# Kernel tuning notes

Hardware: AMD Instinct MI355X
Metric: run time of the kernel (lower is better)

The kernel has to match this reference:

```python
import jax, jax.numpy as jnp
import numpy as np
from jax import lax

T = 2048          # tokens (batch*seq, module flattens to [-1, hidden])
H = 2048          # hidden_size
E = 32            # n_routed_experts
DF = 1024         # moe_intermediate_size
DS = 4096         # moe_shared_expert_intermediate_size
TOP_K = 6         # num_experts_per_tok
N_GROUP = 8
TOPK_GROUP = 4
SCALE = 2.5       # routed_scaling_factor
NORM_TOPK = True


def relu2(x):
    r = jax.nn.relu(x)
    return r * r


def setup_inputs() -> dict:
    key = jax.random.key(0)
    ks = jax.random.split(key, 7)
    s = 0.02
    return {
        "x": jax.random.normal(ks[0], (T, H), dtype=jnp.float32),
        "router_w": jax.random.normal(ks[1], (E, H), dtype=jnp.float32) * s,
        "router_b": jax.random.normal(ks[2], (E,), dtype=jnp.float32) * s,
        "w_up": jax.random.normal(ks[3], (E, H, DF), dtype=jnp.float32) * s,
        "w_down": jax.random.normal(ks[4], (E, DF, H), dtype=jnp.float32) * s,
        "shared_up": jax.random.normal(ks[5], (H, DS), dtype=jnp.float32) * s,
        "shared_down": jax.random.normal(ks[6], (DS, H), dtype=jnp.float32) * s,
    }


def _route(x, router_w, router_b):
    # router in fp32: logits -> sigmoid scores -> group-restricted top-k
    logits = x @ router_w.T                                  # [T, E]
    scores = jax.nn.sigmoid(logits)
    sfc = scores + router_b[None, :]                         # scores_for_choice
    gsize = E // N_GROUP
    grp = sfc.reshape(T, N_GROUP, gsize)
    group_scores = lax.top_k(grp, 2)[0].sum(-1)              # [T, n_group] sum of top-2
    _, gidx = lax.top_k(group_scores, TOPK_GROUP)            # [T, topk_group]
    group_mask = jax.nn.one_hot(gidx, N_GROUP, dtype=sfc.dtype).sum(1)  # [T, n_group]
    score_mask = jnp.repeat(group_mask, gsize, axis=1)       # [T, E]
    masked = jnp.where(score_mask > 0, sfc, 0.0)
    _, tidx = lax.top_k(masked, TOP_K)                       # [T, top_k]
    tw = jnp.take_along_axis(scores, tidx, axis=1)           # gather raw scores
    if NORM_TOPK:
        tw = tw / (tw.sum(-1, keepdims=True) + 1e-20)
    tw = tw * SCALE
    return tidx, tw


def reference(x, router_w, router_b, w_up, w_down, shared_up, shared_down):
    tidx, tw = _route(x, router_w, router_b)
    # dense combine weights [T, E]; equals sum of routed weights per expert
    combine = (jax.nn.one_hot(tidx, E, dtype=tw.dtype) * tw[..., None]).sum(1)
    # routed experts (no bias, so scaling before down_proj == scaling the output)
    h = jnp.einsum('td,edf->tef', x, w_up)                   # [T, E, DF]
    a = relu2(h) * combine[:, :, None]
    moe_out = jnp.einsum('tef,efd->td', a, w_down)           # [T, H]
    shared_out = relu2(x @ shared_up) @ shared_down
    return moe_out + shared_out
```

## Files before the change

### kernel.cpp

```cpp
#include <hip/hip_runtime.h>
#include <hip/hip_bf16.h>
#include <math.h>

#define T_TOK 2048
#define HID   2048
#define NE    32
#define DF    1024
#define DSZ   4096
#define TOPK  6
#define NGRP  8
#define TOPKG 4
#define RSCALE 2.5f
#define EXT_E 36
#define NSLOT 20480

typedef __attribute__((ext_vector_type(8))) short short8;
typedef __attribute__((ext_vector_type(4))) float f32x4;

typedef __attribute__((address_space(1))) const void gv1;
typedef __attribute__((address_space(3))) void lv3;

static __device__ __forceinline__ void gload16(const void* g, void* l) {
    __builtin_amdgcn_global_load_lds((gv1*)g, (lv3*)l, 16, 0, 0);
}

static __device__ __forceinline__ unsigned short f2b(float f) {
    union { float f; unsigned u; } v; v.f = f;
    unsigned r = v.u + 0x7fffu + ((v.u >> 16) & 1u);
    return (unsigned short)(r >> 16);
}

__global__ __launch_bounds__(256)
void router_kernel(const float* __restrict__ x, const float* __restrict__ rw,
                   const float* __restrict__ rb,
                   int* __restrict__ tidx, float* __restrict__ tw,
                   int* __restrict__ counts, unsigned short* __restrict__ xb) {
    __shared__ float xs[HID];
    __shared__ float part[256];
    __shared__ float scores[NE];
    __shared__ float sfc[NE];
    int t = blockIdx.x;
    int tid = threadIdx.x;
    for (int i = tid; i < HID / 4; i += 256) {
        ((float4*)xs)[i] = ((const float4*)(x + (size_t)t * HID))[i];
    }
    __syncthreads();
    {
        float4 a = ((const float4*)xs)[tid * 2];
        float4 b = ((const float4*)xs)[tid * 2 + 1];
        short8 o;
        o[0] = (short)f2b(a.x); o[1] = (short)f2b(a.y); o[2] = (short)f2b(a.z); o[3] = (short)f2b(a.w);
        o[4] = (short)f2b(b.x); o[5] = (short)f2b(b.y); o[6] = (short)f2b(b.z); o[7] = (short)f2b(b.w);
        *(short8*)(xb + (size_t)t * HID + tid * 8) = o;
    }
    int e = tid & 31, ch = tid >> 5;
    const float* w = rw + (size_t)e * HID + ch * 256;
    const float* xv = xs + ch * 256;
    float p = 0.f;
    #pragma unroll 8
    for (int k = 0; k < 256; ++k) p += xv[k] * w[k];
    part[tid] = p;
    __syncthreads();
    if (tid < 32) {
        float l = 0.f;
        #pragma unroll
        for (int c = 0; c < 8; ++c) l += part[c * 32 + tid];
        float s = 1.f / (1.f + expf(-l));
        scores[tid] = s;
        sfc[tid] = s + rb[tid];
    }
    __syncthreads();
    if (tid == 0) {
        float gs[NGRP];
        for (int g = 0; g < NGRP; ++g) {
            float v[4];
            for (int i = 0; i < 4; ++i) v[i] = sfc[g * 4 + i];
            int bi = 0;
            for (int i = 1; i < 4; ++i) if (v[i] > v[bi]) bi = i;
            float m1 = v[bi]; v[bi] = -INFINITY;
            int bj = 0;
            for (int i = 1; i < 4; ++i) if (v[i] > v[bj]) bj = i;
            gs[g] = m1 + v[bj];
        }
        bool gsel[NGRP];
        for (int g = 0; g < NGRP; ++g) gsel[g] = false;
        for (int k = 0; k < TOPKG; ++k) {
            int bi = -1; float b = -INFINITY;
            for (int g = 0; g < NGRP; ++g)
                if (!gsel[g] && gs[g] > b) { b = gs[g]; bi = g; }
            gsel[bi] = true;
        }
        float masked[NE];
        for (int i = 0; i < NE; ++i) masked[i] = gsel[i >> 2] ? sfc[i] : 0.0f;
        int sel[TOPK]; float wv[TOPK]; float wsum = 0.f;
        for (int k = 0; k < TOPK; ++k) {
            int bi = -1; float b = -INFINITY;
            for (int i = 0; i < NE; ++i)
                if (masked[i] > b) { b = masked[i]; bi = i; }
            masked[bi] = -INFINITY;
            sel[k] = bi; wv[k] = scores[bi]; wsum += wv[k];
        }
        float inv = RSCALE / (wsum + 1e-20f);
        for (int k = 0; k < TOPK; ++k) {
            tidx[t * TOPK + k] = sel[k];
            tw[t * TOPK + k] = wv[k] * inv;
            atomicAdd(&counts[sel[k]], 1);
        }
    }
}

__global__ void scan_kernel(const int* __restrict__ counts, int* __restrict__ offsets) {
    if (threadIdx.x == 0) {
        int a = 0;
        for (int e2 = 0; e2 < NE; ++e2) { offsets[e2] = a; a += counts[e2]; }
        offsets[NE] = a;
        for (int j = 1; j <= 4; ++j) offsets[NE + j] = 12288 + j * T_TOK;
    }
}

__global__ void scatter_kernel(const int* __restrict__ tidx, const float* __restrict__ tw,
                               const int* __restrict__ offsets, int* __restrict__ cursors,
                               int* __restrict__ perm, float* __restrict__ pw,
                               int* __restrict__ slot_of) {
    int t = blockIdx.x * blockDim.x + threadIdx.x;
    if (t >= T_TOK) return;
    for (int k = 0; k < TOPK; ++k) {
        int e = tidx[t * TOPK + k];
        int pos = atomicAdd(&cursors[e], 1);
        int slot = offsets[e] + pos;
        perm[slot] = t;
        pw[slot] = tw[t * TOPK + k];
        slot_of[t * TOPK + k] = slot;
    }
    #pragma unroll
    for (int j = 0; j < 4; ++j) {
        int slot = 12288 + j * T_TOK + t;
        perm[slot] = t;
        pw[slot] = 1.0f;
    }
}

static __device__ __forceinline__ void transpose_tile_v2(
        const float* __restrict__ src, unsigned short* __restrict__ dst,
        int rs, int K, int k0, int n0) {
    __shared__ float tile_t[32][132];
    int t = threadIdx.x;
    int kk0 = t >> 3;
    int c4 = (t & 7) * 4;
    #pragma unroll
    for (int p = 0; p < 4; ++p) {
        int kk = kk0 + 32 * p;
        float4 v = *(const float4*)(src + (size_t)(k0 + kk) * rs + n0 + c4);
        tile_t[c4 + 0][kk] = v.x;
        tile_t[c4 + 1][kk] = v.y;
        tile_t[c4 + 2][kk] = v.z;
        tile_t[c4 + 3][kk] = v.w;
    }
    __syncthreads();
    int n = t >> 3;
    int kb = (t & 7) * 8;
    #pragma unroll
    for (int s = 0; s < 2; ++s) {
        int kc = kb + 64 * s;
        float4 a = *(const float4*)&tile_t[n][kc];
        float4 b = *(const float4*)&tile_t[n][kc + 4];
        short8 o;
        o[0] = (short)f2b(a.x); o[1] = (short)f2b(a.y); o[2] = (short)f2b(a.z); o[3] = (short)f2b(a.w);
        o[4] = (short)f2b(b.x); o[5] = (short)f2b(b.y); o[6] = (short)f2b(b.z); o[7] = (short)f2b(b.w);
        *(short8*)(dst + (size_t)(n0 + n) * K + k0 + kc) = o;
    }
}

__global__ __launch_bounds__(256)
void transpose_up_kernel(const float* __restrict__ w_up, const float* __restrict__ sh_up,
                         unsigned short* __restrict__ bufU) {
    int z = blockIdx.z;
    const float* src; int rs;
    if (z < NE) { src = w_up + (size_t)z * HID * DF; rs = DF; }
    else        { src = sh_up + (size_t)(z - NE) * DF; rs = DSZ; }
    transpose_tile_v2(src, bufU + (size_t)z * DF * HID, rs, HID,
                      blockIdx.y * 128, blockIdx.x * 32);
}

__global__ __launch_bounds__(256)
void transpose_dn_kernel(const float* __restrict__ w_dn, const float* __restrict__ sh_dn,
                         unsigned short* __restrict__ bufD) {
    int z = blockIdx.z;
    const float* src = (z < NE) ? (w_dn + (size_t)z * DF * HID)
                                : (sh_dn + (size_t)(z - NE) * DF * HID);
    transpose_tile_v2(src, bufD + (size_t)z * HID * DF, HID, DF,
                      blockIdx.y * 128, blockIdx.x * 32);
}

__global__ __launch_bounds__(256, 2)
void gemm_up_kernel(const unsigned short* __restrict__ xb, const unsigned short* __restrict__ bufU,
                    unsigned short* __restrict__ act, const int* __restrict__ offsets,
                    const int* __restrict__ perm, const float* __restrict__ pw) {
    constexpr int K = HID, N = DF;
    __shared__ __align__(16) char lds[32768];
    char* As = lds;
    char* Bs = lds + 16384;

    int tid = threadIdx.x;
    int lane = tid & 63, wvid = tid >> 6, wr = wvid >> 1, wc = wvid & 1;

    int bz = blockIdx.z;
    int off = offsets[bz], end = offsets[bz + 1];
    int row0 = off + blockIdx.y * 128;
    if (row0 >= end) return;
    int n0 = blockIdx.x * 128;

    int lr = lane >> 3;
    int csrc = (((lane & 7) ^ lr) << 4);
    size_t abyte[4], bbyte[4];
    int ldsoff[4];
    const char* Bb = (const char*)bufU + (size_t)bz * ((size_t)N * K * 2);
    #pragma unroll
    for (int p = 0; p < 4; ++p) {
        int r = p * 32 + wvid * 8 + lr;
        int gr = row0 + r;
        if (gr > end - 1) gr = end - 1;
        abyte[p] = (size_t)perm[gr] * (K * 2);
        bbyte[p] = (size_t)(n0 + r) * (K * 2);
        ldsoff[p] = (p * 32 + wvid * 8) * 128;
    }

    f32x4 acc[4][4] = {};
    for (int k0 = 0; k0 < K; k0 += 64) {
        __syncthreads();
        #pragma unroll
        for (int p = 0; p < 4; ++p) {
            gload16((const char*)xb + abyte[p] + k0 * 2 + csrc, As + ldsoff[p]);
            gload16(Bb + bbyte[p] + k0 * 2 + csrc, Bs + ldsoff[p]);
        }
        __syncthreads();
        #pragma unroll
        for (int ks = 0; ks < 2; ++ks) {
            int kg = lane >> 4, r16 = lane & 15;
            short8 af[4], bfr[4];
            #pragma unroll
            for (int m = 0; m < 4; ++m) {
                int r = wr * 64 + m * 16 + r16;
                af[m] = *(const short8*)(As + r * 128 + ((ks * 64 + kg * 16) ^ ((r & 7) << 4)));
            }
            #pragma unroll
            for (int n = 0; n < 4; ++n) {
                int c = wc * 64 + n * 16 + r16;
                bfr[n] = *(const short8*)(Bs + c * 128 + ((ks * 64 + kg * 16) ^ ((c & 7) << 4)));
            }
            #pragma unroll
            for (int m = 0; m < 4; ++m)
                #pragma unroll
                for (int n = 0; n < 4; ++n)
                    acc[m][n] = __builtin_amdgcn_mfma_f32_16x16x32_bf16(af[m], bfr[n], acc[m][n], 0, 0, 0);
        }
    }

    int r16 = lane & 15, rg = lane >> 4;
    #pragma unroll
    for (int m = 0; m < 4; ++m) {
        #pragma unroll
        for (int j = 0; j < 4; ++j) {
            int rr = row0 + wr * 64 + m * 16 + rg * 4 + j;
            if (rr < end) {
                float scale = pw[rr];
                #pragma unroll
                for (int n = 0; n < 4; ++n) {
                    int cc = n0 + wc * 64 + n * 16 + r16;
                    float v = acc[m][n][j];
                    v = v > 0.f ? v * v : 0.f;
                    act[(size_t)rr * N + cc] = f2b(v * scale);
                }
            }
        }
    }
}

__global__ __launch_bounds__(256, 2)
void gemm_down_kernel(const unsigned short* __restrict__ act, const unsigned short* __restrict__ bufD,
                      float* __restrict__ slotout, const int* __restrict__ offsets) {
    constexpr int K = DF, N = HID;
    __shared__ __align__(16) char lds[32768];
    char* As = lds;
    char* Bs = lds + 16384;

    int tid = threadIdx.x;
    int lane = tid & 63, wvid = tid >> 6, wr = wvid >> 1, wc = wvid & 1;

    int bz = blockIdx.z;
    int off = offsets[bz], end = offsets[bz + 1];
    int row0 = off + blockIdx.y * 128;
    if (row0 >= end) return;
    int n0 = blockIdx.x * 128;

    int lr = lane >> 3;
    int csrc = (((lane & 7) ^ lr) << 4);
    size_t abyte[4], bbyte[4];
    int ldsoff[4];
    const char* Bb = (const char*)bufD + (size_t)bz * ((size_t)N * K * 2);
    #pragma unroll
    for (int p = 0; p < 4; ++p) {
        int r = p * 32 + wvid * 8 + lr;
        int gr = row0 + r;
        if (gr > end - 1) gr = end - 1;
        abyte[p] = (size_t)gr * (K * 2);
        bbyte[p] = (size_t)(n0 + r) * (K * 2);
        ldsoff[p] = (p * 32 + wvid * 8) * 128;
    }

    f32x4 acc[4][4] = {};
    for (int k0 = 0; k0 < K; k0 += 64) {
        __syncthreads();
        #pragma unroll
        for (int p = 0; p < 4; ++p) {
            gload16((const char*)act + abyte[p] + k0 * 2 + csrc, As + ldsoff[p]);
            gload16(Bb + bbyte[p] + k0 * 2 + csrc, Bs + ldsoff[p]);
        }
        __syncthreads();
        #pragma unroll
        for (int ks = 0; ks < 2; ++ks) {
            int kg = lane >> 4, r16 = lane & 15;
            short8 af[4], bfr[4];
            #pragma unroll
            for (int m = 0; m < 4; ++m) {
                int r = wr * 64 + m * 16 + r16;
                af[m] = *(const short8*)(As + r * 128 + ((ks * 64 + kg * 16) ^ ((r & 7) << 4)));
            }
            #pragma unroll
            for (int n = 0; n < 4; ++n) {
                int c = wc * 64 + n * 16 + r16;
                bfr[n] = *(const short8*)(Bs + c * 128 + ((ks * 64 + kg * 16) ^ ((c & 7) << 4)));
            }
            #pragma unroll
            for (int m = 0; m < 4; ++m)
                #pragma unroll
                for (int n = 0; n < 4; ++n)
                    acc[m][n] = __builtin_amdgcn_mfma_f32_16x16x32_bf16(af[m], bfr[n], acc[m][n], 0, 0, 0);
        }
    }

    int r16 = lane & 15, rg = lane >> 4;
    #pragma unroll
    for (int m = 0; m < 4; ++m) {
        #pragma unroll
        for (int j = 0; j < 4; ++j) {
            int rr = row0 + wr * 64 + m * 16 + rg * 4 + j;
            if (rr < end) {
                #pragma unroll
                for (int n = 0; n < 4; ++n) {
                    int cc = n0 + wc * 64 + n * 16 + r16;
                    slotout[(size_t)rr * N + cc] = acc[m][n][j];
                }
            }
        }
    }
}

__global__ void combine_kernel(const float* __restrict__ slotout, const int* __restrict__ slot_of,
                               float* __restrict__ out) {
    int t = blockIdx.x, tid = threadIdx.x;
    int s[10];
    #pragma unroll
    for (int k = 0; k < TOPK; ++k) s[k] = slot_of[t * TOPK + k];
    #pragma unroll
    for (int j = 0; j < 4; ++j) s[TOPK + j] = 12288 + j * T_TOK + t;
    #pragma unroll
    for (int p = 0; p < 2; ++p) {
        int c = (p * 256 + tid) * 4;
        float4 a = {0.f, 0.f, 0.f, 0.f};
        #pragma unroll
        for (int k = 0; k < 10; ++k) {
            float4 v = *(const float4*)(slotout + (size_t)s[k] * HID + c);
            a.x += v.x; a.y += v.y; a.z += v.z; a.w += v.w;
        }
        *(float4*)(out + (size_t)t * HID + c) = a;
    }
}

extern "C" void kernel_launch(void* const* d_in, const int* in_sizes, int n_in,
                              void* d_out, int out_size, void* d_ws, size_t ws_size,
                              hipStream_t stream) {
    const float* x     = (const float*)d_in[0];
    const float* rw    = (const float*)d_in[1];
    const float* rb    = (const float*)d_in[2];
    const float* w_up  = (const float*)d_in[3];
    const float* w_dn  = (const float*)d_in[4];
    const float* sh_up = (const float*)d_in[5];
    const float* sh_dn = (const float*)d_in[6];
    float* out = (float*)d_out;
    char* ws = (char*)d_ws;

    int*   counts  = (int*)(ws);
    int*   cursors = (int*)(ws + 128);
    int*   offsets = (int*)(ws + 256);
    int*   tidx    = (int*)(ws + 1024);
    float* tw      = (float*)(ws + 50176);
    int*   slot_of = (int*)(ws + 99328);
    int*   perm    = (int*)(ws + 148480);
    float* pw      = (float*)(ws + 230400);
    unsigned short* xb   = (unsigned short*)(ws + 312320);
    unsigned short* act  = (unsigned short*)(ws + 8700928);
    unsigned short* bufU = (unsigned short*)(ws + 50643968);
    unsigned short* bufD = (unsigned short*)(ws + 201638912);
    float* slotout       = (float*)(ws + 352633856);

    hipMemsetAsync(ws, 0, 256, stream);

    router_kernel<<<T_TOK, 256, 0, stream>>>(x, rw, rb, tidx, tw, counts, xb);
    scan_kernel<<<1, 64, 0, stream>>>(counts, offsets);
    scatter_kernel<<<(T_TOK + 255) / 256, 256, 0, stream>>>(tidx, tw, offsets, cursors,
                                                            perm, pw, slot_of);

    transpose_up_kernel<<<dim3(32, 16, EXT_E), 256, 0, stream>>>(w_up, sh_up, bufU);
    gemm_up_kernel<<<dim3(DF / 128, T_TOK / 128, EXT_E), 256, 0, stream>>>(
        xb, bufU, act, offsets, perm, pw);

    transpose_dn_kernel<<<dim3(64, 8, EXT_E), 256, 0, stream>>>(w_dn, sh_dn, bufD);
    gemm_down_kernel<<<dim3(HID / 128, T_TOK / 128, EXT_E), 256, 0, stream>>>(
        act, bufD, slotout, offsets);

    combine_kernel<<<T_TOK, 256, 0, stream>>>(slotout, slot_of, out);
}
```

Baseline: 600.5 us.

## Double-buffer LDS in MoE GEMMs and rewrite weight transpose without shared memory

```diff
diff --git a/kernel.cpp b/kernel.cpp
--- a/kernel.cpp
+++ b/kernel.cpp
@@ -140,34 +140,19 @@
     }
 }
 
-static __device__ __forceinline__ void transpose_tile_v2(
+static __device__ __forceinline__ void transpose_col32(
         const float* __restrict__ src, unsigned short* __restrict__ dst,
-        int rs, int K, int k0, int n0) {
-    __shared__ float tile_t[32][132];
-    int t = threadIdx.x;
-    int kk0 = t >> 3;
-    int c4 = (t & 7) * 4;
-    #pragma unroll
-    for (int p = 0; p < 4; ++p) {
-        int kk = kk0 + 32 * p;
-        float4 v = *(const float4*)(src + (size_t)(k0 + kk) * rs + n0 + c4);
-        tile_t[c4 + 0][kk] = v.x;
-        tile_t[c4 + 1][kk] = v.y;
-        tile_t[c4 + 2][kk] = v.z;
-        tile_t[c4 + 3][kk] = v.w;
-    }
-    __syncthreads();
-    int n = t >> 3;
-    int kb = (t & 7) * 8;
-    #pragma unroll
-    for (int s = 0; s < 2; ++s) {
-        int kc = kb + 64 * s;
-        float4 a = *(const float4*)&tile_t[n][kc];
-        float4 b = *(const float4*)&tile_t[n][kc + 4];
+        int rs, int K, int k0, int n) {
+    float v[32];
+    #pragma unroll
+    for (int p = 0; p < 32; ++p)
+        v[p] = src[(size_t)(k0 + p) * rs + n];
+    #pragma unroll
+    for (int q = 0; q < 4; ++q) {
         short8 o;
-        o[0] = (short)f2b(a.x); o[1] = (short)f2b(a.y); o[2] = (short)f2b(a.z); o[3] = (short)f2b(a.w);
-        o[4] = (short)f2b(b.x); o[5] = (short)f2b(b.y); o[6] = (short)f2b(b.z); o[7] = (short)f2b(b.w);
-        *(short8*)(dst + (size_t)(n0 + n) * K + k0 + kc) = o;
+        #pragma unroll
+        for (int i = 0; i < 8; ++i) o[i] = (short)f2b(v[q * 8 + i]);
+        *(short8*)(dst + (size_t)n * K + k0 + q * 8) = o;
     }
 }
 
@@ -178,8 +163,8 @@
     const float* src; int rs;
     if (z < NE) { src = w_up + (size_t)z * HID * DF; rs = DF; }
     else        { src = sh_up + (size_t)(z - NE) * DF; rs = DSZ; }
-    transpose_tile_v2(src, bufU + (size_t)z * DF * HID, rs, HID,
-                      blockIdx.y * 128, blockIdx.x * 32);
+    transpose_col32(src, bufU + (size_t)z * DF * HID, rs, HID,
+                    blockIdx.y * 32, blockIdx.x * 256 + threadIdx.x);
 }
 
 __global__ __launch_bounds__(256)
@@ -188,8 +173,8 @@
     int z = blockIdx.z;
     const float* src = (z < NE) ? (w_dn + (size_t)z * DF * HID)
                                 : (sh_dn + (size_t)(z - NE) * DF * HID);
-    transpose_tile_v2(src, bufD + (size_t)z * HID * DF, HID, DF,
-                      blockIdx.y * 128, blockIdx.x * 32);
+    transpose_col32(src, bufD + (size_t)z * HID * DF, HID, DF,
+                    blockIdx.y * 32, blockIdx.x * 256 + threadIdx.x);
 }
 
 __global__ __launch_bounds__(256, 2)
@@ -197,9 +182,7 @@
                     unsigned short* __restrict__ act, const int* __restrict__ offsets,
                     const int* __restrict__ perm, const float* __restrict__ pw) {
     constexpr int K = HID, N = DF;
-    __shared__ __align__(16) char lds[32768];
-    char* As = lds;
-    char* Bs = lds + 16384;
+    __shared__ __align__(16) char lds[65536];
 
     int tid = threadIdx.x;
     int lane = tid & 63, wvid = tid >> 6, wr = wvid >> 1, wc = wvid & 1;
@@ -226,14 +209,27 @@
     }
 
     f32x4 acc[4][4] = {};
-    for (int k0 = 0; k0 < K; k0 += 64) {
-        __syncthreads();
-        #pragma unroll
-        for (int p = 0; p < 4; ++p) {
-            gload16((const char*)xb + abyte[p] + k0 * 2 + csrc, As + ldsoff[p]);
-            gload16(Bb + bbyte[p] + k0 * 2 + csrc, Bs + ldsoff[p]);
-        }
-        __syncthreads();
+    constexpr int NT = K / 64;
+    int cur = 0;
+    #pragma unroll
+    for (int p = 0; p < 4; ++p) {
+        gload16((const char*)xb + abyte[p] + csrc, lds + ldsoff[p]);
+        gload16(Bb + bbyte[p] + csrc, lds + 16384 + ldsoff[p]);
+    }
+    __syncthreads();
+
+    for (int t = 0; t < NT; ++t) {
+        char* As = lds + cur * 32768;
+        char* Bs = As + 16384;
+        if (t + 1 < NT) {
+            int k2 = (t + 1) * 128;
+            char* Ad = lds + (cur ^ 1) * 32768;
+            #pragma unroll
+            for (int p = 0; p < 4; ++p) {
+                gload16((const char*)xb + abyte[p] + k2 + csrc, Ad + ldsoff[p]);
+                gload16(Bb + bbyte[p] + k2 + csrc, Ad + 16384 + ldsoff[p]);
+            }
+        }
         #pragma unroll
         for (int ks = 0; ks < 2; ++ks) {
             int kg = lane >> 4, r16 = lane & 15;
@@ -254,6 +250,8 @@
                 for (int n = 0; n < 4; ++n)
                     acc[m][n] = __builtin_amdgcn_mfma_f32_16x16x32_bf16(af[m], bfr[n], acc[m][n], 0, 0, 0);
         }
+        __syncthreads();
+        cur ^= 1;
     }
 
     int r16 = lane & 15, rg = lane >> 4;
@@ -280,9 +278,7 @@
 void gemm_down_kernel(const unsigned short* __restrict__ act, const unsigned short* __restrict__ bufD,
                       float* __restrict__ slotout, const int* __restrict__ offsets) {
     constexpr int K = DF, N = HID;
-    __shared__ __align__(16) char lds[32768];
-    char* As = lds;
-    char* Bs = lds + 16384;
+    __shared__ __align__(16) char lds[65536];
 
     int tid = threadIdx.x;
     int lane = tid & 63, wvid = tid >> 6, wr = wvid >> 1, wc = wvid & 1;
@@ -309,14 +305,27 @@
     }
 
     f32x4 acc[4][4] = {};
-    for (int k0 = 0; k0 < K; k0 += 64) {
-        __syncthreads();
-        #pragma unroll
-        for (int p = 0; p < 4; ++p) {
-            gload16((const char*)act + abyte[p] + k0 * 2 + csrc, As + ldsoff[p]);
-            gload16(Bb + bbyte[p] + k0 * 2 + csrc, Bs + ldsoff[p]);
-        }
-        __syncthreads();
+    constexpr int NT = K / 64;
+    int cur = 0;
+    #pragma unroll
+    for (int p = 0; p < 4; ++p) {
+        gload16((const char*)act + abyte[p] + csrc, lds + ldsoff[p]);
+        gload16(Bb + bbyte[p] + csrc, lds + 16384 + ldsoff[p]);
+    }
+    __syncthreads();
+
+    for (int t = 0; t < NT; ++t) {
+        char* As = lds + cur * 32768;
+        char* Bs = As + 16384;
+        if (t + 1 < NT) {
+            int k2 = (t + 1) * 128;
+            char* Ad = lds + (cur ^ 1) * 32768;
+            #pragma unroll
+            for (int p = 0; p < 4; ++p) {
+                gload16((const char*)act + abyte[p] + k2 + csrc, Ad + ldsoff[p]);
+                gload16(Bb + bbyte[p] + k2 + csrc, Ad + 16384 + ldsoff[p]);
+            }
+        }
         #pragma unroll
         for (int ks = 0; ks < 2; ++ks) {
             int kg = lane >> 4, r16 = lane & 15;
@@ -337,6 +346,8 @@
                 for (int n = 0; n < 4; ++n)
                     acc[m][n] = __builtin_amdgcn_mfma_f32_16x16x32_bf16(af[m], bfr[n], acc[m][n], 0, 0, 0);
         }
+        __syncthreads();
+        cur ^= 1;
     }
 
     int r16 = lane & 15, rg = lane >> 4;
@@ -411,11 +422,11 @@
     scatter_kernel<<<(T_TOK + 255) / 256, 256, 0, stream>>>(tidx, tw, offsets, cursors,
                                                             perm, pw, slot_of);
 
-    transpose_up_kernel<<<dim3(32, 16, EXT_E), 256, 0, stream>>>(w_up, sh_up, bufU);
+    transpose_up_kernel<<<dim3(DF / 256, HID / 32, EXT_E), 256, 0, stream>>>(w_up, sh_up, bufU);
     gemm_up_kernel<<<dim3(DF / 128, T_TOK / 128, EXT_E), 256, 0, stream>>>(
         xb, bufU, act, offsets, perm, pw);
 
-    transpose_dn_kernel<<<dim3(64, 8, EXT_E), 256, 0, stream>>>(w_dn, sh_dn, bufD);
+    transpose_dn_kernel<<<dim3(HID / 256, DF / 32, EXT_E), 256, 0, stream>>>(w_dn, sh_dn, bufD);
     gemm_down_kernel<<<dim3(HID / 128, T_TOK / 128, EXT_E), 256, 0, stream>>>(
         act, bufD, slotout, offsets);
 
```

Result: slower. 726.5 us (+21.0%).

## Merge weight transposes into one kernel and store down-proj slot outputs as bf16

Applied to the files above, without the earlier changes.

```diff
diff --git a/kernel.cpp b/kernel.cpp
--- a/kernel.cpp
+++ b/kernel.cpp
@@ -28,6 +28,11 @@
     union { float f; unsigned u; } v; v.f = f;
     unsigned r = v.u + 0x7fffu + ((v.u >> 16) & 1u);
     return (unsigned short)(r >> 16);
+}
+
+static __device__ __forceinline__ float b2f(unsigned short b) {
+    union { float f; unsigned u; } v; v.u = ((unsigned)b) << 16;
+    return v.f;
 }
 
 __global__ __launch_bounds__(256)
@@ -140,56 +145,52 @@
     }
 }
 
-static __device__ __forceinline__ void transpose_tile_v2(
+static __device__ __forceinline__ void transpose_tile64(
         const float* __restrict__ src, unsigned short* __restrict__ dst,
-        int rs, int K, int k0, int n0) {
-    __shared__ float tile_t[32][132];
+        int rs, int Kd, int k0, int n0) {
+    __shared__ float tl[64][65];
     int t = threadIdx.x;
-    int kk0 = t >> 3;
-    int c4 = (t & 7) * 4;
+    int r0 = t >> 4;
+    int c4 = (t & 15) * 4;
     #pragma unroll
     for (int p = 0; p < 4; ++p) {
-        int kk = kk0 + 32 * p;
-        float4 v = *(const float4*)(src + (size_t)(k0 + kk) * rs + n0 + c4);
-        tile_t[c4 + 0][kk] = v.x;
-        tile_t[c4 + 1][kk] = v.y;
-        tile_t[c4 + 2][kk] = v.z;
-        tile_t[c4 + 3][kk] = v.w;
+        int r = r0 + p * 16;
+        float4 v = *(const float4*)(src + (size_t)(k0 + r) * rs + n0 + c4);
+        tl[c4 + 0][r] = v.x;
+        tl[c4 + 1][r] = v.y;
+        tl[c4 + 2][r] = v.z;
+        tl[c4 + 3][r] = v.w;
     }
     __syncthreads();
-    int n = t >> 3;
-    int kb = (t & 7) * 8;
-    #pragma unroll
-    for (int s = 0; s < 2; ++s) {
-        int kc = kb + 64 * s;
-        float4 a = *(const float4*)&tile_t[n][kc];
-        float4 b = *(const float4*)&tile_t[n][kc + 4];
-        short8 o;
-        o[0] = (short)f2b(a.x); o[1] = (short)f2b(a.y); o[2] = (short)f2b(a.z); o[3] = (short)f2b(a.w);
-        o[4] = (short)f2b(b.x); o[5] = (short)f2b(b.y); o[6] = (short)f2b(b.z); o[7] = (short)f2b(b.w);
-        *(short8*)(dst + (size_t)(n0 + n) * K + k0 + kc) = o;
-    }
+    int n = t >> 2;
+    int kq = (t & 3) * 16;
+    unsigned short o[16];
+    #pragma unroll
+    for (int i = 0; i < 16; ++i) o[i] = f2b(tl[n][kq + i]);
+    unsigned short* d = dst + (size_t)(n0 + n) * Kd + k0 + kq;
+    *(short8*)(d) = *(short8*)&o[0];
+    *(short8*)(d + 8) = *(short8*)&o[8];
 }
 
 __global__ __launch_bounds__(256)
-void transpose_up_kernel(const float* __restrict__ w_up, const float* __restrict__ sh_up,
-                         unsigned short* __restrict__ bufU) {
-    int z = blockIdx.z;
-    const float* src; int rs;
-    if (z < NE) { src = w_up + (size_t)z * HID * DF; rs = DF; }
-    else        { src = sh_up + (size_t)(z - NE) * DF; rs = DSZ; }
-    transpose_tile_v2(src, bufU + (size_t)z * DF * HID, rs, HID,
-                      blockIdx.y * 128, blockIdx.x * 32);
-}
-
-__global__ __launch_bounds__(256)
-void transpose_dn_kernel(const float* __restrict__ w_dn, const float* __restrict__ sh_dn,
-                         unsigned short* __restrict__ bufD) {
-    int z = blockIdx.z;
-    const float* src = (z < NE) ? (w_dn + (size_t)z * DF * HID)
-                                : (sh_dn + (size_t)(z - NE) * DF * HID);
-    transpose_tile_v2(src, bufD + (size_t)z * HID * DF, HID, DF,
-                      blockIdx.y * 128, blockIdx.x * 32);
+void transpose_all_kernel(const float* __restrict__ w_up, const float* __restrict__ sh_up,
+                          const float* __restrict__ w_dn, const float* __restrict__ sh_dn,
+                          unsigned short* __restrict__ bufU, unsigned short* __restrict__ bufD) {
+    int z = blockIdx.y;
+    int tile = blockIdx.x;
+    if (z < EXT_E) {
+        const float* src; int rs;
+        if (z < NE) { src = w_up + (size_t)z * HID * DF; rs = DF; }
+        else        { src = sh_up + (size_t)(z - NE) * DF; rs = DSZ; }
+        int tn = tile & 15, tk = tile >> 4;
+        transpose_tile64(src, bufU + (size_t)z * DF * HID, rs, HID, tk * 64, tn * 64);
+    } else {
+        int zz = z - EXT_E;
+        const float* src = (zz < NE) ? (w_dn + (size_t)zz * DF * HID)
+                                     : (sh_dn + (size_t)(zz - NE) * DF * HID);
+        int tn = tile & 31, tk = tile >> 5;
+        transpose_tile64(src, bufD + (size_t)zz * HID * DF, HID, DF, tk * 64, tn * 64);
+    }
 }
 
 __global__ __launch_bounds__(256, 2)
@@ -278,7 +279,7 @@
 
 __global__ __launch_bounds__(256, 2)
 void gemm_down_kernel(const unsigned short* __restrict__ act, const unsigned short* __restrict__ bufD,
-                      float* __restrict__ slotout, const int* __restrict__ offsets) {
+                      unsigned short* __restrict__ slotout, const int* __restrict__ offsets) {
     constexpr int K = DF, N = HID;
     __shared__ __align__(16) char lds[32768];
     char* As = lds;
@@ -349,14 +350,15 @@
                 #pragma unroll
                 for (int n = 0; n < 4; ++n) {
                     int cc = n0 + wc * 64 + n * 16 + r16;
-                    slotout[(size_t)rr * N + cc] = acc[m][n][j];
+                    slotout[(size_t)rr * N + cc] = f2b(acc[m][n][j]);
                 }
             }
         }
     }
 }
 
-__global__ void combine_kernel(const float* __restrict__ slotout, const int* __restrict__ slot_of,
+__global__ void combine_kernel(const unsigned short* __restrict__ slotout,
+                               const int* __restrict__ slot_of,
                                float* __restrict__ out) {
     int t = blockIdx.x, tid = threadIdx.x;
     int s[10];
@@ -364,17 +366,16 @@
     for (int k = 0; k < TOPK; ++k) s[k] = slot_of[t * TOPK + k];
     #pragma unroll
     for (int j = 0; j < 4; ++j) s[TOPK + j] = 12288 + j * T_TOK + t;
-    #pragma unroll
-    for (int p = 0; p < 2; ++p) {
-        int c = (p * 256 + tid) * 4;
-        float4 a = {0.f, 0.f, 0.f, 0.f};
-        #pragma unroll
-        for (int k = 0; k < 10; ++k) {
-            float4 v = *(const float4*)(slotout + (size_t)s[k] * HID + c);
-            a.x += v.x; a.y += v.y; a.z += v.z; a.w += v.w;
-        }
-        *(float4*)(out + (size_t)t * HID + c) = a;
-    }
+    int c = tid * 8;
+    float a[8] = {0.f, 0.f, 0.f, 0.f, 0.f, 0.f, 0.f, 0.f};
+    #pragma unroll
+    for (int k = 0; k < 10; ++k) {
+        short8 v = *(const short8*)(slotout + (size_t)s[k] * HID + c);
+        #pragma unroll
+        for (int i = 0; i < 8; ++i) a[i] += b2f((unsigned short)v[i]);
+    }
+    *(float4*)(out + (size_t)t * HID + c) = make_float4(a[0], a[1], a[2], a[3]);
+    *(float4*)(out + (size_t)t * HID + c + 4) = make_float4(a[4], a[5], a[6], a[7]);
 }
 
 extern "C" void kernel_launch(void* const* d_in, const int* in_sizes, int n_in,
@@ -402,7 +403,7 @@
     unsigned short* act  = (unsigned short*)(ws + 8700928);
     unsigned short* bufU = (unsigned short*)(ws + 50643968);
     unsigned short* bufD = (unsigned short*)(ws + 201638912);
-    float* slotout       = (float*)(ws + 352633856);
+    unsigned short* slotout = (unsigned short*)(ws + 352633856);
 
     hipMemsetAsync(ws, 0, 256, stream);
 
@@ -411,11 +412,12 @@
     scatter_kernel<<<(T_TOK + 255) / 256, 256, 0, stream>>>(tidx, tw, offsets, cursors,
                                                             perm, pw, slot_of);
 
-    transpose_up_kernel<<<dim3(32, 16, EXT_E), 256, 0, stream>>>(w_up, sh_up, bufU);
+    transpose_all_kernel<<<dim3(512, 2 * EXT_E), 256, 0, stream>>>(
+        w_up, sh_up, w_dn, sh_dn, bufU, bufD);
+
     gemm_up_kernel<<<dim3(DF / 128, T_TOK / 128, EXT_E), 256, 0, stream>>>(
         xb, bufU, act, offsets, perm, pw);
 
-    transpose_dn_kernel<<<dim3(64, 8, EXT_E), 256, 0, stream>>>(w_dn, sh_dn, bufD);
     gemm_down_kernel<<<dim3(HID / 128, T_TOK / 128, EXT_E), 256, 0, stream>>>(
         act, bufD, slotout, offsets);
 
```

New measurement: 572.8 us. 1.05x faster.
